# Kernel optimization log

Measured on AMD Instinct MI355X. Metric: run time of the kernel, lower is better.

## Reference

```python
import jax, jax.numpy as jnp
import numpy as np

B, CIN, NH, W, L, K = 16, 64, 64, 32, 4, 5
EPS = 1e-5
FORGET_BIAS = 1.0


def conv(x, w, b=None):
    # x: [B,C,H,W], w: [O,I,k,k] -> SAME padding, stride 1 (NCHW)
    y = jax.lax.conv_general_dilated(x, w, (1, 1), 'SAME',
                                     dimension_numbers=('NCHW', 'OIHW', 'NCHW'))
    if b is not None:
        y = y + b[None, :, None, None]
    return y


def ln(x, g, b):
    # torch LayerNorm([C,W,W]): normalize each sample over (C,H,W)
    m = jnp.mean(x, axis=(1, 2, 3), keepdims=True)
    v = jnp.mean((x - m) ** 2, axis=(1, 2, 3), keepdims=True)
    return (x - m) * jax.lax.rsqrt(v + EPS) * g[None] + b[None]


def attn_channel(q, kv):
    # q: [B,C,W,H], kv: [B,L,C,W,H]
    b, c, w, h = q.shape
    qf = q.reshape(b, c, w * h)                 # [B,C,HW]
    kf = kv.reshape(b, -1, w * h)               # [B,L*C,HW]
    a = jax.nn.softmax(jnp.einsum('bcp,blp->bcl', qf, kf), axis=2)  # [B,C,L*C]
    out = jnp.einsum('bcl,blp->bcp', a, kf)     # [B,C,HW]
    return out.reshape(b, c, w, h)


def attn_spatial(q, kv):
    # q: [B,C,W,H], kv: [B,L,C,W,H]
    b, c, w, h = q.shape
    qf = q.reshape(b, c, w * h).transpose(0, 2, 1)          # [B,HW,C]
    kf = kv.transpose(0, 1, 3, 4, 2).reshape(b, -1, c)      # [B,L*HW,C]
    a = jax.nn.softmax(jnp.einsum('bpc,bqc->bpq', qf, kf), axis=2)  # [B,HW,L*HW]
    out = jnp.einsum('bpq,bqc->bpc', a, kf)                 # [B,HW,C]
    return out.reshape(b, w, h, c).transpose(0, 3, 1, 2)


def setup_inputs() -> dict:
    key = jax.random.key(0)
    ks = iter(jax.random.split(key, 64))
    rn = lambda shape, s=1.0: jax.random.normal(next(ks), shape, jnp.float32) * s
    ones = lambda shape: jnp.ones(shape, jnp.float32)
    zeros = lambda shape: jnp.zeros(shape, jnp.float32)
    s = 0.02
    d = {}
    d['x_t'] = rn((B, CIN, W, W))
    d['h_t'] = rn((B, NH, W, W))
    d['c_t'] = rn((B, NH, W, W))
    d['c_historys'] = rn((B, L, NH, W, W))
    d['m_t'] = rn((B, NH, W, W))
    d['w_x'] = rn((7 * NH, CIN, K, K), s); d['ln_x_g'] = ones((7 * NH, W, W)); d['ln_x_b'] = zeros((7 * NH, W, W))
    d['w_h'] = rn((4 * NH, NH, K, K), s);  d['ln_h_g'] = ones((4 * NH, W, W)); d['ln_h_b'] = zeros((4 * NH, W, W))
    d['w_m'] = rn((3 * NH, NH, K, K), s);  d['ln_m_g'] = ones((3 * NH, W, W)); d['ln_m_b'] = zeros((3 * NH, W, W))
    d['w_o'] = rn((NH, 2 * NH, K, K), s);  d['ln_o_g'] = ones((NH, W, W));     d['ln_o_b'] = zeros((NH, W, W))
    d['w_last'] = rn((NH, 2 * NH, 1, 1), s)
    d['s_norm_g'] = ones((NH, W, W)); d['s_norm_b'] = zeros((NH, W, W))
    d['c_norm_g'] = ones((NH, W, W)); d['c_norm_b'] = zeros((NH, W, W))
    d['ca_w1'] = rn((NH, NH, K, K), s); d['ca_b1'] = zeros((NH,))
    d['ca_ln_g'] = ones((NH, W, W));    d['ca_ln_b'] = zeros((NH, W, W))
    d['ca_w2'] = rn((NH, NH, 1, 1), s); d['ca_b2'] = zeros((NH,))
    d['sa_w1'] = rn((NH, NH, K, K), s)
    d['sa_ln_g'] = ones((NH, W, W));    d['sa_ln_b'] = zeros((NH, W, W))
    d['sa_w2'] = rn((NH, NH, 1, 1), s)
    d['attn_w'] = rn((NH, NH, 1, 1), s)
    return d


def reference(x_t, h_t, c_t, c_historys, m_t,
              w_x, ln_x_g, ln_x_b, w_h, ln_h_g, ln_h_b, w_m, ln_m_g, ln_m_b,
              w_o, ln_o_g, ln_o_b, w_last,
              s_norm_g, s_norm_b, c_norm_g, c_norm_b,
              ca_w1, ca_b1, ca_ln_g, ca_ln_b, ca_w2, ca_b2,
              sa_w1, sa_ln_g, sa_ln_b, sa_w2, attn_w):
    x_concat = ln(conv(x_t, w_x), ln_x_g, ln_x_b)
    h_concat = ln(conv(h_t, w_h), ln_h_g, ln_h_b)
    m_concat = ln(conv(m_t, w_m), ln_m_g, ln_m_b)
    (i_x, f_x, g_x, i_xp, f_xp, g_xp, o_x) = jnp.split(x_concat, 7, axis=1)
    (i_h, f_h, g_h, o_h) = jnp.split(h_concat, 4, axis=1)
    (i_m, f_m, g_m) = jnp.split(m_concat, 3, axis=1)

    i_t = jax.nn.sigmoid(i_x + i_h)
    f_t = jax.nn.sigmoid(f_x + f_h + FORGET_BIAS)
    g_t = jnp.tanh(g_x + g_h)

    # attn_sum_fussion(c_t, query=f_t, keys=c_historys, values=c_historys)
    sp = ln(c_t + attn_spatial(f_t, c_historys), s_norm_g, s_norm_b)
    ch = ln(c_t + attn_channel(f_t, c_historys), c_norm_g, c_norm_b)
    s_a = conv(jax.nn.relu(ln(conv(sp, sa_w1), sa_ln_g, sa_ln_b)), sa_w2)
    c_a = conv(jax.nn.relu(ln(conv(ch, ca_w1, ca_b1), ca_ln_g, ca_ln_b)), ca_w2, ca_b2)
    attn = conv(s_a + c_a, attn_w)
    c_new = attn + i_t * g_t

    i_tp = jax.nn.sigmoid(i_xp + i_m)
    f_tp = jax.nn.sigmoid(f_xp + f_m + FORGET_BIAS)
    g_tp = jnp.tanh(g_xp + g_m)
    m_new = f_tp * m_t + i_tp * g_tp

    mem = jnp.concatenate((c_new, m_new), axis=1)
    o_t = jax.nn.sigmoid(o_x + o_h + ln(conv(mem, w_o), ln_o_g, ln_o_b))
    h_new = o_t * jnp.tanh(conv(mem, w_last))
    return h_new, c_new, m_new
```

## Files before the change

### kernel.cpp

```cpp
#include <hip/hip_runtime.h>
#include <hip/hip_bf16.h>

#define N1 (1u << 20)

typedef __attribute__((ext_vector_type(8))) short s8v;
typedef __attribute__((ext_vector_type(4))) float f4v;

static __device__ __forceinline__ float sigm(float x){ return 1.f/(1.f + __expf(-x)); }
static __device__ __forceinline__ float tanh_(float x){ return 1.f - 2.f/(__expf(2.f*x) + 1.f); }

static __device__ __forceinline__ ushort f2b(float f){
  union { float f; uint u; } x; x.f = f;
  uint r = x.u + 0x7FFFu + ((x.u >> 16) & 1u);
  return (ushort)(r >> 16);
}

static __device__ __forceinline__ void red_atomic2(float s, float q, float* d, int b, int t){
  #pragma unroll
  for (int m = 32; m; m >>= 1){ s += __shfl_xor(s, m); q += __shfl_xor(q, m); }
  if ((t & 63) == 0){ atomicAdd(&d[b*2], s); atomicAdd(&d[b*2+1], q); }
}

__global__ void k_zero(float* __restrict__ p){ p[threadIdx.x] = 0.f; }

__global__ __launch_bounds__(256) void k_wprep3(
    const float* __restrict__ sA, ushort* __restrict__ dA, int CoA, int CiA, int nA,
    const float* __restrict__ sB, ushort* __restrict__ dB, int CoB, int CiB, int nB,
    const float* __restrict__ sC, ushort* __restrict__ dC, int CoC, int CiC, int nC)
{
  int idx = blockIdx.x*256 + threadIdx.x;
  const float* s; ushort* d; int Co, Ci;
  if (idx < nA){ s=sA; d=dA; Co=CoA; Ci=CiA; }
  else if ((idx -= nA) < nB){ s=sB; d=dB; Co=CoB; Ci=CiB; }
  else if ((idx -= nB) < nC){ s=sC; d=dC; Co=CoC; Ci=CiC; }
  else return;
  const int ci32 = idx & 31;
  const int r  = idx >> 5;
  const int co = r % Co;
  const int r2 = r / Co;
  const int tap = r2 % 25, cc = r2 / 25;
  d[idx] = f2b(s[((size_t)(co*Ci + (cc<<5) + ci32))*25 + tap]);
}

struct PT { const float* s; ushort* d; const float* st; const float* g; const float* bb; };

__global__ __launch_bounds__(256) void k_prepT3(PT ja, PT jb, PT jc, int n0, int n1, float invN)
{
  const int lp = blockIdx.y;
  PT j; int pl;
  if (lp < n0){ j = ja; pl = lp; }
  else if (lp < n0 + n1){ j = jb; pl = lp - n0; }
  else { j = jc; pl = lp - n0 - n1; }
  const float* sp = j.s + ((size_t)pl << 16);
  float mean = 0.f, rstd = 0.f;
  if (j.st){
    float s0 = j.st[pl*2], s1 = j.st[pl*2+1];
    mean = s0*invN; rstd = rsqrtf(s1*invN - mean*mean + 1e-5f);
  }
  const int p0 = blockIdx.x << 6;
  __shared__ __align__(16) float T[64][68];
  const int t = threadIdx.x, c = t >> 2, g4 = t & 3;
  #pragma unroll
  for (int i = 0; i < 4; ++i){
    const int px = (g4 << 4) + (i << 2);
    float4 f = *(const float4*)(sp + ((size_t)c << 10) + p0 + px);
    if (j.st){
      const size_t li = ((size_t)c << 10) + p0 + px;
      float4 gv = *(const float4*)(j.g + li);
      float4 bv = *(const float4*)(j.bb + li);
      f.x = (f.x - mean)*rstd*gv.x + bv.x;
      f.y = (f.y - mean)*rstd*gv.y + bv.y;
      f.z = (f.z - mean)*rstd*gv.z + bv.z;
      f.w = (f.w - mean)*rstd*gv.w + bv.w;
    }
    *(float4*)&T[c][px] = f;
  }
  __syncthreads();
  const int p = t >> 2, c0 = (t & 3) << 4;
  uint w4[8];
  #pragma unroll
  for (int k = 0; k < 8; ++k){
    ushort lo = f2b(T[c0 + 2*k][p]);
    ushort hi = f2b(T[c0 + 2*k + 1][p]);
    w4[k] = (uint)lo | ((uint)hi << 16);
  }
  ushort* dst = j.d + ((((size_t)pl << 10) + p0 + p) << 6) + c0;
  *(uint4*)(dst)     = *(uint4*)&w4[0];
  *(uint4*)(dst + 8) = *(uint4*)&w4[4];
}

__global__ __launch_bounds__(256) void k_prepTm(const float* __restrict__ src, ushort* __restrict__ dT)
{
  const int lp = blockIdx.y;
  const int p0 = blockIdx.x << 6;
  const float* sp = src + ((size_t)lp << 16);
  __shared__ __align__(16) float T[64][68];
  const int t = threadIdx.x, c = t >> 2, g4 = t & 3;
  #pragma unroll
  for (int i = 0; i < 4; ++i){
    const int px = (g4 << 4) + (i << 2);
    *(float4*)&T[c][px] = *(const float4*)(sp + ((size_t)c << 10) + p0 + px);
  }
  __syncthreads();
  const int p = t >> 2, c0 = (t & 3) << 4;
  uint w4[8];
  #pragma unroll
  for (int k = 0; k < 8; ++k)
    w4[k] = (uint)f2b(T[c0 + 2*k][p]) | ((uint)f2b(T[c0 + 2*k + 1][p]) << 16);
  ushort* dst = dT + ((((size_t)(lp >> 1) << 10) + p0 + p) << 7) + ((lp & 1) << 6) + c0;
  *(uint4*)(dst)     = *(uint4*)&w4[0];
  *(uint4*)(dst + 8) = *(uint4*)&w4[4];
}

struct Seg {
  const ushort* inT; const ushort* w; const float* bias;
  float* out; float* ostat;
  int Cin, Cout;
};
struct Segs3 { Seg s[3]; int b1, b2; };

template<int MT>
__global__ __launch_bounds__(256, MT==4 ? 3 : 4) void k_convX(Segs3 Sg)
{
  constexpr int CO = MT*16;
  const int b = blockIdx.y;
  const int cog = blockIdx.x >> 2, pxblk = blockIdx.x & 3;
  const int si = (cog >= Sg.b1) + (cog >= Sg.b2);
  const Seg sg = Sg.s[si];
  const int base = si == 0 ? 0 : (si == 1 ? Sg.b1 : Sg.b2);
  const int co0 = (cog - base) * CO;
  const int r0 = pxblk << 3;
  const int t = threadIdx.x, w = t >> 6, l = t & 63;
  const int lane16 = l & 15, quad = l >> 4;
  const int lofs = (lane16 << 5) + (quad << 3);

  __shared__ __align__(16) ushort S_[4][12][36][8];

  f4v acc[MT][4];
  #pragma unroll
  for (int mi = 0; mi < MT; ++mi)
    #pragma unroll
    for (int n = 0; n < 4; ++n) acc[mi][n] = (f4v){0.f,0.f,0.f,0.f};

  const int ncc = sg.Cin >> 5;
  for (int cc = 0; cc < ncc; ++cc){
    __syncthreads();
    for (int idx = t; idx < 432; idx += 256){
      const int row = idx / 36, col = idx - row*36;
      const int ir = r0 - 2 + row, ic = col - 2;
      uint4 pk[4] = {make_uint4(0,0,0,0),make_uint4(0,0,0,0),make_uint4(0,0,0,0),make_uint4(0,0,0,0)};
      if ((unsigned)ir < 32u && (unsigned)ic < 32u){
        const ushort* bp = sg.inT + ((size_t)((b << 10) + (ir << 5) + ic)) * sg.Cin + (cc << 5);
        #pragma unroll
        for (int q = 0; q < 4; ++q) pk[q] = *(const uint4*)(bp + (q << 3));
      }
      #pragma unroll
      for (int q = 0; q < 4; ++q) *(uint4*)&S_[q][row][col][0] = pk[q];
    }
    __syncthreads();
    #pragma unroll
    for (int dy = 0; dy < 5; ++dy){
      #pragma unroll
      for (int dx = 0; dx < 5; ++dx){
        const ushort* wp = sg.w + (((size_t)((cc*25 + dy*5 + dx)*sg.Cout + co0)) << 5) + lofs;
        s8v a[MT];
        #pragma unroll
        for (int mi = 0; mi < MT; ++mi)
          a[mi] = *(const s8v*)(wp + mi*512);
        #pragma unroll
        for (int n = 0; n < 4; ++n){
          const int srow = (w << 1) + (n >> 1) + dy;
          const int col = ((n & 1) << 4) + lane16 + dx;
          s8v bb = *(const s8v*)&S_[quad][srow][col][0];
          #pragma unroll
          for (int mi = 0; mi < MT; ++mi)
            acc[mi][n] = __builtin_amdgcn_mfma_f32_16x16x32_bf16(a[mi], bb, acc[mi][n], 0, 0, 0);
        }
      }
    }
  }
  float lsum = 0.f, lsq = 0.f;
  #pragma unroll
  for (int mi = 0; mi < MT; ++mi){
    const int co = co0 + mi*16 + (quad << 2);
    #pragma unroll
    for (int n = 0; n < 4; ++n){
      const int row = r0 + (w << 1) + (n >> 1);
      const int col = ((n & 1) << 4) + lane16;
      #pragma unroll
      for (int i = 0; i < 4; ++i){
        float v = acc[mi][n][i] + (sg.bias ? sg.bias[co+i] : 0.f);
        sg.out[(((size_t)(b*sg.Cout + co + i)) << 10) + (row << 5) + col] = v;
        lsum += v; lsq += v*v;
      }
    }
  }
  if (sg.ostat) red_atomic2(lsum, lsq, sg.ostat, b, t);
}

__global__ __launch_bounds__(256) void k_prep(const float* __restrict__ src,
                                              ushort* __restrict__ outC,
                                              ushort* __restrict__ outT)
{
  const int plane = blockIdx.y;
  const int p0 = blockIdx.x << 6;
  const float* sp = src + ((size_t)plane << 16);
  __shared__ __align__(16) float T[64][68];
  const int t = threadIdx.x, c = t >> 2, g = t & 3;
  #pragma unroll
  for (int i = 0; i < 4; ++i){
    float4 f = *(const float4*)(sp + ((size_t)c << 10) + p0 + (g << 4) + (i << 2));
    *(float4*)&T[c][(g << 4) + (i << 2)] = f;
    if (outC){
      uint2 pk2;
      pk2.x = (uint)f2b(f.x) | ((uint)f2b(f.y) << 16);
      pk2.y = (uint)f2b(f.z) | ((uint)f2b(f.w) << 16);
      *(uint2*)(outC + ((((size_t)plane << 6) + c) << 10) + p0 + (g << 4) + (i << 2)) = pk2;
    }
  }
  __syncthreads();
  const int p = t >> 2, c0 = (t & 3) << 4;
  uint w4[8];
  #pragma unroll
  for (int k = 0; k < 8; ++k){
    ushort lo = f2b(T[c0 + 2*k][p]);
    ushort hi = f2b(T[c0 + 2*k + 1][p]);
    w4[k] = (uint)lo | ((uint)hi << 16);
  }
  ushort* dst = outT + ((((size_t)plane << 10) + p0 + p) << 6) + c0;
  *(uint4*)(dst)     = *(uint4*)&w4[0];
  *(uint4*)(dst + 8) = *(uint4*)&w4[4];
}

__global__ __launch_bounds__(256) void k_gates(
    const float* __restrict__ bufx, const float* __restrict__ bufh, const float* __restrict__ bufm,
    const float* __restrict__ lnxg, const float* __restrict__ lnxb,
    const float* __restrict__ lnhg, const float* __restrict__ lnhb,
    const float* __restrict__ lnmg, const float* __restrict__ lnmb,
    const float* __restrict__ m_t, const float* __restrict__ stats,
    float* __restrict__ ft, float* __restrict__ ig, float* __restrict__ osum,
    float* __restrict__ memo, float* __restrict__ out_m)
{
  const int idx = blockIdx.x*256 + threadIdx.x;
  const int b = idx >> 16, rem = idx & 65535;
  const int c = rem >> 10, p = rem & 1023;

  float mx = stats[b*2]      * (1.f/458752.f);
  float vx = stats[b*2+1]    * (1.f/458752.f) - mx*mx;  float rx = rsqrtf(vx + 1e-5f);
  float mh = stats[32+b*2]   * (1.f/262144.f);
  float vh = stats[32+b*2+1] * (1.f/262144.f) - mh*mh;  float rh = rsqrtf(vh + 1e-5f);
  float mm = stats[64+b*2]   * (1.f/196608.f);
  float vm = stats[64+b*2+1] * (1.f/196608.f) - mm*mm;  float rm = rsqrtf(vm + 1e-5f);

  auto LX = [&](int k){
    size_t ch = (size_t)k*64 + c; size_t gi = ((size_t)b*448 + ch)*1024 + p; size_t li = ch*1024 + p;
    return (bufx[gi] - mx)*rx*lnxg[li] + lnxb[li]; };
  auto LH = [&](int k){
    size_t ch = (size_t)k*64 + c; size_t gi = ((size_t)b*256 + ch)*1024 + p; size_t li = ch*1024 + p;
    return (bufh[gi] - mh)*rh*lnhg[li] + lnhb[li]; };
  auto LM = [&](int k){
    size_t ch = (size_t)k*64 + c; size_t gi = ((size_t)b*192 + ch)*1024 + p; size_t li = ch*1024 + p;
    return (bufm[gi] - mm)*rm*lnmg[li] + lnmb[li]; };

  float i_t = sigm(LX(0) + LH(0));
  float f_t = sigm(LX(1) + LH(1) + 1.f);
  float g_t = tanh_(LX(2) + LH(2));
  float i_p = sigm(LX(3) + LM(0));
  float f_p = sigm(LX(4) + LM(1) + 1.f);
  float g_p = tanh_(LX(5) + LM(2));
  float ox = LX(6), oh = LH(3);

  ft[idx]   = f_t;
  ig[idx]   = i_t * g_t;
  osum[idx] = ox + oh;
  float mn = f_p * m_t[idx] + i_p * g_p;
  out_m[idx] = mn;
  memo[((size_t)(b*128 + 64 + c) << 10) + p] = mn;
}

__global__ __launch_bounds__(256) void k_spat_mfma(
    const ushort* __restrict__ qT, const ushort* __restrict__ kvC, const ushort* __restrict__ kvT,
    const float* __restrict__ c_t, float* __restrict__ sp_raw, float* __restrict__ stats)
{
  const int p0 = blockIdx.x << 6, b = blockIdx.y;
  const int t = threadIdx.x, w = t >> 6, l = t & 63;
  const int lane16 = l & 15, quad = l >> 4;
  __shared__ __align__(16) ushort Kt[64][72];
  __shared__ __align__(16) ushort Kc[64][72];
  __shared__ __align__(16) ushort Eb[64][72];
  __shared__ __align__(16) float  XO[64][65];

  s8v qa0, qa1;
  {
    const ushort* qr = qT + ((((size_t)b << 10) + p0 + (w << 4) + lane16) << 6) + (quad << 3);
    qa0 = *(const s8v*)(qr);
    qa1 = *(const s8v*)(qr + 32);
  }
  f4v o0 = {0.f,0.f,0.f,0.f}, o1 = o0, o2 = o0, o3 = o0, dacc = o0;
  const short oneb = (short)0x3F80;
  const s8v ones = { oneb, oneb, oneb, oneb, oneb, oneb, oneb, oneb };

  const int r = t >> 2, g4 = (t & 3) << 4;
  for (int chunk = 0; chunk < 64; ++chunk){
    const int lidx = chunk >> 4, pk = (chunk & 15) << 6;
    __syncthreads();
    {
      const ushort* sc = kvC + ((((size_t)(b*4 + lidx) << 6) + r) << 10) + pk + g4;
      *(uint4*)&Kc[r][g4]     = *(const uint4*)(sc);
      *(uint4*)&Kc[r][g4 + 8] = *(const uint4*)(sc + 8);
      const ushort* st = kvT + ((((size_t)(b*4 + lidx) << 10) + pk + r) << 6) + g4;
      *(uint4*)&Kt[r][g4]     = *(const uint4*)(st);
      *(uint4*)&Kt[r][g4 + 8] = *(const uint4*)(st + 8);
    }
    __syncthreads();
    #pragma unroll
    for (int nt = 0; nt < 4; ++nt){
      const ushort* bt = &Kt[(nt << 4) + lane16][quad << 3];
      s8v b0 = *(const s8v*)(bt);
      s8v b1 = *(const s8v*)(bt + 32);
      f4v s = {0.f,0.f,0.f,0.f};
      s = __builtin_amdgcn_mfma_f32_16x16x32_bf16(qa0, b0, s, 0, 0, 0);
      s = __builtin_amdgcn_mfma_f32_16x16x32_bf16(qa1, b1, s, 0, 0, 0);
      #pragma unroll
      for (int i = 0; i < 4; ++i){
        float e = __expf(s[i] - 12.f);
        Eb[(w << 4) + (quad << 2) + i][(nt << 4) + lane16] = f2b(e);
      }
    }
    __syncthreads();
    #pragma unroll
    for (int ks = 0; ks < 2; ++ks){
      s8v ea = *(const s8v*)&Eb[(w << 4) + lane16][(ks << 5) + (quad << 3)];
      dacc = __builtin_amdgcn_mfma_f32_16x16x32_bf16(ea, ones, dacc, 0, 0, 0);
      s8v bc0 = *(const s8v*)&Kc[ 0 + lane16][(ks << 5) + (quad << 3)];
      s8v bc1 = *(const s8v*)&Kc[16 + lane16][(ks << 5) + (quad << 3)];
      s8v bc2 = *(const s8v*)&Kc[32 + lane16][(ks << 5) + (quad << 3)];
      s8v bc3 = *(const s8v*)&Kc[48 + lane16][(ks << 5) + (quad << 3)];
      o0 = __builtin_amdgcn_mfma_f32_16x16x32_bf16(ea, bc0, o0, 0, 0, 0);
      o1 = __builtin_amdgcn_mfma_f32_16x16x32_bf16(ea, bc1, o1, 0, 0, 0);
      o2 = __builtin_amdgcn_mfma_f32_16x16x32_bf16(ea, bc2, o2, 0, 0, 0);
// ... 229 lines not shown
  float acc2[4][4] = {};
  for (int c2 = 0; c2 < 64; ++c2){
    float wv[4], mv[4];
    *(float4*)wv = *(const float4*)&Wl[c2][4*tc];
    *(float4*)mv = *(const float4*)&Ms[c2][4*tp];
    #pragma unroll
    for (int i = 0; i < 4; ++i)
      #pragma unroll
      for (int j = 0; j < 4; ++j)
        acc2[i][j] = fmaf(wv[i], mv[j], acc2[i][j]);
  }
  #pragma unroll
  for (int i = 0; i < 4; ++i)
    #pragma unroll
    for (int j = 0; j < 4; ++j){
      size_t gi = ((size_t)b << 16) + ((size_t)(4*tc + i) << 10) + p0 + 4*tp + j;
      float v = acc2[i][j] + ig[gi];
      out_c[gi] = v;
      memo[((size_t)(b*128 + 4*tc + i) << 10) + p0 + 4*tp + j] = v;
    }
}

__global__ __launch_bounds__(256) void k_final(
    const float* __restrict__ memo, const float* __restrict__ wlast,
    const float* __restrict__ bufo, const float* __restrict__ osum,
    const float* __restrict__ stats_o, const float* __restrict__ lnog, const float* __restrict__ lnob,
    float* __restrict__ out_h)
{
  const int p0 = blockIdx.x << 6, b = blockIdx.y, t = threadIdx.x;
  const int tc = t & 15, tp = t >> 4;
  __shared__ __align__(16) float Msh[64][68];
  __shared__ __align__(16) float Wt[64][68];
  float acc[4][4] = {};
  #pragma unroll
  for (int half = 0; half < 2; ++half){
    __syncthreads();
    {
      const int j = t & 63, c0 = t >> 6;
      for (int ci = c0; ci < 64; ci += 4)
        Msh[ci][j] = memo[((size_t)(b*128 + half*64 + ci) << 10) + p0 + j];
      const int ci2 = t & 63, co0 = t >> 6;
      for (int co = co0; co < 64; co += 4) Wt[ci2][co] = wlast[((size_t)co << 7) + half*64 + ci2];
    }
    __syncthreads();
    for (int ci = 0; ci < 64; ++ci){
      float wv[4], mv[4];
      *(float4*)wv = *(const float4*)&Wt[ci][4*tc];
      *(float4*)mv = *(const float4*)&Msh[ci][4*tp];
      #pragma unroll
      for (int i = 0; i < 4; ++i)
        #pragma unroll
        for (int j = 0; j < 4; ++j)
          acc[i][j] = fmaf(wv[i], mv[j], acc[i][j]);
    }
  }
  float mean = stats_o[b*2]*(1.f/65536.f);
  float var  = stats_o[b*2+1]*(1.f/65536.f) - mean*mean;
  float rstd = rsqrtf(var + 1e-5f);
  #pragma unroll
  for (int i = 0; i < 4; ++i)
    #pragma unroll
    for (int j = 0; j < 4; ++j){
      const int co = 4*tc + i, p = p0 + 4*tp + j;
      size_t gi = ((size_t)b << 16) + ((size_t)co << 10) + p;
      size_t li = ((size_t)co << 10) + p;
      float lno = (bufo[gi] - mean)*rstd*lnog[li] + lnob[li];
      float o = sigm(osum[gi] + lno);
      out_h[gi] = o * tanh_(acc[i][j]);
    }
}

extern "C" void kernel_launch(void* const* d_in, const int* in_sizes, int n_in,
                              void* d_out, int out_size, void* d_ws, size_t ws_size,
                              hipStream_t stream)
{
  const float* x_t   = (const float*)d_in[0];
  const float* h_t   = (const float*)d_in[1];
  const float* c_t   = (const float*)d_in[2];
  const float* chist = (const float*)d_in[3];
  const float* m_t   = (const float*)d_in[4];
  const float* w_x   = (const float*)d_in[5];
  const float* lnxg  = (const float*)d_in[6];
  const float* lnxb  = (const float*)d_in[7];
  const float* w_h   = (const float*)d_in[8];
  const float* lnhg  = (const float*)d_in[9];
  const float* lnhb  = (const float*)d_in[10];
  const float* w_m   = (const float*)d_in[11];
  const float* lnmg  = (const float*)d_in[12];
  const float* lnmb  = (const float*)d_in[13];
  const float* w_o   = (const float*)d_in[14];
  const float* lnog  = (const float*)d_in[15];
  const float* lnob  = (const float*)d_in[16];
  const float* w_last= (const float*)d_in[17];
  const float* sng   = (const float*)d_in[18];
  const float* snb   = (const float*)d_in[19];
  const float* cng   = (const float*)d_in[20];
  const float* cnb   = (const float*)d_in[21];
  const float* ca_w1 = (const float*)d_in[22];
  const float* ca_b1 = (const float*)d_in[23];
  const float* calng = (const float*)d_in[24];
  const float* calnb = (const float*)d_in[25];
  const float* ca_w2 = (const float*)d_in[26];
  const float* ca_b2 = (const float*)d_in[27];
  const float* sa_w1 = (const float*)d_in[28];
  const float* salng = (const float*)d_in[29];
  const float* salnb = (const float*)d_in[30];
  const float* sa_w2 = (const float*)d_in[31];
  const float* attn_w= (const float*)d_in[32];

  float* out = (float*)d_out;
  float* ws  = (float*)d_ws;

  float* stats = ws;
  float* bufx  = ws + 1024;
  float* bufh  = bufx + 7*(size_t)N1;
  float* bufm  = bufh + 4*(size_t)N1;
  float* ft    = bufm + 3*(size_t)N1;
  float* ig    = ft   + (size_t)N1;
  float* osum  = ig   + (size_t)N1;
  float* memo  = osum + (size_t)N1;
  float* sp    = bufx;
  float* ch    = bufx + (size_t)N1;
  float* samid = bufx + 2*(size_t)N1;
  float* camid = bufx + 3*(size_t)N1;
  float* bufo  = bufx + 4*(size_t)N1;
  float* chl   = bufx + 5*(size_t)N1;
  ushort* kvC  = (ushort*)bufh;
  ushort* kvT  = kvC + 4*(size_t)N1;
  ushort* qT   = (ushort*)bufm;
  ushort* ftC  = qT + (size_t)N1;

  ushort* xT   = (ushort*)memo;
  ushort* hT   = xT + (size_t)N1;
  ushort* mT   = hT + (size_t)N1;
  ushort* spT  = ftC + (size_t)N1;
  ushort* chT  = spT + (size_t)N1;
  ushort* memoT = (ushort*)bufx;

  ushort* wbx = (ushort*)ft;
  ushort* wbh = wbx + 716800;
  ushort* wbm = wbh + 409600;
  ushort* wbo  = (ushort*)(chl + 262144);
  ushort* wbsa = wbo + 204800;
  ushort* wbca = wbsa + 102400;
  ushort* chlb = wbca + 102400;

  float* out_h = out;
  float* out_c = out + (size_t)N1;
  float* out_m = out + 2*(size_t)N1;

  k_zero<<<dim3(1), dim3(256), 0, stream>>>(stats);

  k_wprep3<<<dim3(5600), dim3(256), 0, stream>>>(
      w_x, wbx, 448, 64, 716800,
      w_h, wbh, 256, 64, 409600,
      w_m, wbm, 192, 64, 307200);

  {
    PT jx{ x_t, xT, nullptr, nullptr, nullptr };
    PT jh{ h_t, hT, nullptr, nullptr, nullptr };
    PT jm{ m_t, mT, nullptr, nullptr, nullptr };
    k_prepT3<<<dim3(16,48), dim3(256), 0, stream>>>(jx, jh, jm, 16, 16, 0.f);
  }

  {
    Segs3 XHM;
    XHM.s[0] = Seg{ xT, wbx, nullptr, bufx, stats+0,  64, 448 };
    XHM.s[1] = Seg{ hT, wbh, nullptr, bufh, stats+32, 64, 256 };
    XHM.s[2] = Seg{ mT, wbm, nullptr, bufm, stats+64, 64, 192 };
    XHM.b1 = 7; XHM.b2 = 11;
    k_convX<4><<<dim3(56,16), dim3(256), 0, stream>>>(XHM);
  }

  k_gates<<<dim3(4096), dim3(256), 0, stream>>>(bufx, bufh, bufm, lnxg, lnxb, lnhg, lnhb,
                                                lnmg, lnmb, m_t, stats,
                                                ft, ig, osum, memo, out_m);

  k_wprep3<<<dim3(1600), dim3(256), 0, stream>>>(
      w_o,   wbo,  64, 128, 204800,
      sa_w1, wbsa, 64,  64, 102400,
      ca_w1, wbca, 64,  64, 102400);

  k_prep<<<dim3(16,64), dim3(256), 0, stream>>>(chist, kvC, kvT);
  k_prep<<<dim3(16,16), dim3(256), 0, stream>>>(ft, ftC, qT);

  k_spat_mfma<<<dim3(16,16), dim3(256), 0, stream>>>(qT, kvC, kvT, c_t, sp, stats+96);
  k_chlog_m<<<dim3(2,16), dim3(256), 0, stream>>>(ftC, kvC, chl);
  k_chsm  <<<dim3(256),  dim3(256), 0, stream>>>(chl, chlb);
  k_chout_m<<<dim3(8,16), dim3(256), 0, stream>>>(chlb, kvT, c_t, ch, stats+128);

  {
    PT js{ sp, spT, stats+96,  sng, snb };
    PT jc{ ch, chT, stats+128, cng, cnb };
    k_prepT3<<<dim3(16,32), dim3(256), 0, stream>>>(js, jc, js, 16, 16, 1.f/65536.f);
  }

  {
    Segs3 SC;
    SC.s[0] = Seg{ spT, wbsa, nullptr, samid, stats+160, 64, 64 };
    SC.s[1] = Seg{ chT, wbca, ca_b1,   camid, stats+192, 64, 64 };
    SC.s[2] = SC.s[1];
    SC.b1 = 2; SC.b2 = 1000;
    k_convX<2><<<dim3(16,16), dim3(256), 0, stream>>>(SC);
  }

  k_attnfinal<<<dim3(16,16), dim3(256), 0, stream>>>(samid, camid, stats+160, stats+192,
                                                     salng, salnb, calng, calnb,
                                                     sa_w2, ca_w2, ca_b2, attn_w,
                                                     ig, out_c, memo);

  k_prepTm<<<dim3(16,32), dim3(256), 0, stream>>>(memo, memoT);

  {
    Segs3 O;
    O.s[0] = Seg{ memoT, wbo, nullptr, bufo, stats+224, 128, 64 };
    O.s[1] = O.s[0]; O.s[2] = O.s[0];
    O.b1 = 1000; O.b2 = 1000;
    k_convX<2><<<dim3(8,16), dim3(256), 0, stream>>>(O);
  }

  k_final<<<dim3(16,16), dim3(256), 0, stream>>>(memo, w_last, bufo, osum, stats+224,
                                                 lnog, lnob, out_h);
}
```

Measured before the change: 550.6 us.

## Stage conv weights through double-buffered LDS with register prefetch per kernel row

Conv weights are now stored as [tap][Cout][Cin] instead of the chunked layout. Each dy row's weights for the block's output channels are cooperatively loaded into a double-buffered shared-memory tile, and the next row is prefetched into registers while MFMAs run on the current one. This replaces per-wave direct global weight loads, which several waves repeated, with shared LDS reads. In exchange it adds a __syncthreads per dy row and more LDS and register use, and the launch-bounds occupancy hint is lowered to match.

```diff
diff --git a/kernel.cpp b/kernel.cpp
--- a/kernel.cpp
+++ b/kernel.cpp
@@ -34,12 +34,8 @@
   else if ((idx -= nA) < nB){ s=sB; d=dB; Co=CoB; Ci=CiB; }
   else if ((idx -= nB) < nC){ s=sC; d=dC; Co=CoC; Ci=CiC; }
   else return;
-  const int ci32 = idx & 31;
-  const int r  = idx >> 5;
-  const int co = r % Co;
-  const int r2 = r / Co;
-  const int tap = r2 % 25, cc = r2 / 25;
-  d[idx] = f2b(s[((size_t)(co*Ci + (cc<<5) + ci32))*25 + tap]);
+  int ci = idx % Ci; int r = idx / Ci; int co = r % Co; int tap = r / Co;
+  d[idx] = f2b(s[((size_t)(co*Ci + ci))*25 + tap]);
 }
 
 struct PT { const float* s; ushort* d; const float* st; const float* g; const float* bb; };
@@ -120,9 +116,13 @@
 struct Segs3 { Seg s[3]; int b1, b2; };
 
 template<int MT>
-__global__ __launch_bounds__(256, MT==4 ? 3 : 4) void k_convX(Segs3 Sg)
-{
-  constexpr int CO = MT*16;
+__global__ __launch_bounds__(256, MT==4 ? 2 : 3) void k_convX(Segs3 Sg)
+{
+  constexpr int CO   = MT*16;
+  constexpr int NW   = 5*CO*4;
+  constexpr int ITW  = (NW + 255) / 256;
+  constexpr int DXSH = (MT == 4 ? 8 : 7);
+
   const int b = blockIdx.y;
   const int cog = blockIdx.x >> 2, pxblk = blockIdx.x & 3;
   const int si = (cog >= Sg.b1) + (cog >= Sg.b2);
@@ -132,15 +132,25 @@
   const int r0 = pxblk << 3;
   const int t = threadIdx.x, w = t >> 6, l = t & 63;
   const int lane16 = l & 15, quad = l >> 4;
-  const int lofs = (lane16 << 5) + (quad << 3);
 
   __shared__ __align__(16) ushort S_[4][12][36][8];
+  __shared__ __align__(16) ushort W_[2][5*CO*32];
 
   f4v acc[MT][4];
   #pragma unroll
   for (int mi = 0; mi < MT; ++mi)
     #pragma unroll
     for (int n = 0; n < 4; ++n) acc[mi][n] = (f4v){0.f,0.f,0.f,0.f};
+
+  size_t woff0[ITW];
+  #pragma unroll
+  for (int it = 0; it < ITW; ++it){
+    const int u = t + it*256;
+    const int l16u = u & 15, qu = (u >> 4) & 3;
+    const int miu = (u >> 6) & (MT - 1), dxu = u >> DXSH;
+    woff0[it] = ((size_t)(dxu*sg.Cout + co0 + miu*16 + l16u))*sg.Cin + (qu << 3);
+  }
+  const size_t wdy = (size_t)5 * sg.Cout * sg.Cin;
 
   const int ncc = sg.Cin >> 5;
   for (int cc = 0; cc < ncc; ++cc){
@@ -157,16 +167,35 @@
       #pragma unroll
       for (int q = 0; q < 4; ++q) *(uint4*)&S_[q][row][col][0] = pk[q];
     }
+    {
+      uint4 wreg[ITW];
+      #pragma unroll
+      for (int it = 0; it < ITW; ++it)
+        if (ITW*256 == NW || t + it*256 < NW)
+          wreg[it] = *(const uint4*)(sg.w + woff0[it] + (cc << 5));
+      #pragma unroll
+      for (int it = 0; it < ITW; ++it)
+        if (ITW*256 == NW || t + it*256 < NW)
+          *(uint4*)&W_[0][(size_t)(t + it*256) * 8] = wreg[it];
+    }
     __syncthreads();
     #pragma unroll
     for (int dy = 0; dy < 5; ++dy){
+      uint4 nreg[ITW];
+      if (dy < 4){
+        #pragma unroll
+        for (int it = 0; it < ITW; ++it)
+          if (ITW*256 == NW || t + it*256 < NW)
+            nreg[it] = *(const uint4*)(sg.w + woff0[it] + (size_t)(dy+1)*wdy + (cc << 5));
+      }
       #pragma unroll
       for (int dx = 0; dx < 5; ++dx){
-        const ushort* wp = sg.w + (((size_t)((cc*25 + dy*5 + dx)*sg.Cout + co0)) << 5) + lofs;
         s8v a[MT];
         #pragma unroll
-        for (int mi = 0; mi < MT; ++mi)
-          a[mi] = *(const s8v*)(wp + mi*512);
+        for (int mi = 0; mi < MT; ++mi){
+          const int au = ((((dx*MT + mi) << 2) + quad) << 4) + lane16;
+          a[mi] = *(const s8v*)&W_[dy & 1][au << 3];
+        }
         #pragma unroll
         for (int n = 0; n < 4; ++n){
           const int srow = (w << 1) + (n >> 1) + dy;
@@ -177,6 +206,13 @@
             acc[mi][n] = __builtin_amdgcn_mfma_f32_16x16x32_bf16(a[mi], bb, acc[mi][n], 0, 0, 0);
         }
       }
+      if (dy < 4){
+        #pragma unroll
+        for (int it = 0; it < ITW; ++it)
+          if (ITW*256 == NW || t + it*256 < NW)
+            *(uint4*)&W_[(dy+1) & 1][(size_t)(t + it*256) * 8] = nreg[it];
+      }
+      __syncthreads();
     }
   }
   float lsum = 0.f, lsq = 0.f;
```

New measurement: 519.0 us. -5.7%, faster.

## Re-layout conv weights and activations, prefetch weight fragments, split small convs finer

Applied to the files above, without the earlier changes.

Weights are now packed per output-channel tile with taps innermost, so each block reads a contiguous region. Activations are stored in 8-channel group planes, which makes each LDS fill a single 16-byte load per unit. The conv loop double-buffers the A (weight) fragments one tap ahead to hide global-load latency behind the MFMAs. The smaller convs use 4 rows per block, doubling the grid to improve occupancy at the cost of more halo reloads. This rests on a new layout contract between the prep kernels and the conv kernel, and every consumer of these buffers must agree with it.

```diff
diff --git a/kernel.cpp b/kernel.cpp
--- a/kernel.cpp
+++ b/kernel.cpp
@@ -24,22 +24,28 @@
 __global__ void k_zero(float* __restrict__ p){ p[threadIdx.x] = 0.f; }
 
 __global__ __launch_bounds__(256) void k_wprep3(
-    const float* __restrict__ sA, ushort* __restrict__ dA, int CoA, int CiA, int nA,
-    const float* __restrict__ sB, ushort* __restrict__ dB, int CoB, int CiB, int nB,
-    const float* __restrict__ sC, ushort* __restrict__ dC, int CoC, int CiC, int nC)
+    const float* __restrict__ sA, ushort* __restrict__ dA, int CoA, int CiA, int COA, int nA,
+    const float* __restrict__ sB, ushort* __restrict__ dB, int CoB, int CiB, int COB, int nB,
+    const float* __restrict__ sC, ushort* __restrict__ dC, int CoC, int CiC, int COC, int nC)
 {
   int idx = blockIdx.x*256 + threadIdx.x;
-  const float* s; ushort* d; int Co, Ci;
-  if (idx < nA){ s=sA; d=dA; Co=CoA; Ci=CiA; }
-  else if ((idx -= nA) < nB){ s=sB; d=dB; Co=CoB; Ci=CiB; }
-  else if ((idx -= nB) < nC){ s=sC; d=dC; Co=CoC; Ci=CiC; }
+  const float* s; ushort* d; int Co, Ci, CO;
+  if (idx < nA){ s=sA; d=dA; Co=CoA; Ci=CiA; CO=COA; }
+  else if ((idx -= nA) < nB){ s=sB; d=dB; Co=CoB; Ci=CiB; CO=COB; }
+  else if ((idx -= nB) < nC){ s=sC; d=dC; Co=CoC; Ci=CiC; CO=COC; }
   else return;
-  const int ci32 = idx & 31;
-  const int r  = idx >> 5;
-  const int co = r % Co;
-  const int r2 = r / Co;
-  const int tap = r2 % 25, cc = r2 / 25;
-  d[idx] = f2b(s[((size_t)(co*Ci + (cc<<5) + ci32))*25 + tap]);
+  const int ci8 = idx & 7;
+  int u = idx >> 3;
+  const int q = u & 3; u >>= 2;
+  const int cl = u % CO; u /= CO;
+  const int dx = u % 5;  u /= 5;
+  const int dy = u % 5;  u /= 5;
+  const int nCot = Co / CO;
+  const int cot = u % nCot;
+  const int cc  = u / nCot;
+  const int co = cot*CO + cl;
+  const int ci = (cc << 5) + (q << 3) + ci8;
+  d[idx] = f2b(s[((size_t)(co*Ci + ci))*25 + dy*5 + dx]);
 }
 
 struct PT { const float* s; ushort* d; const float* st; const float* g; const float* bb; };
@@ -84,9 +90,11 @@
     ushort hi = f2b(T[c0 + 2*k + 1][p]);
     w4[k] = (uint)lo | ((uint)hi << 16);
   }
-  ushort* dst = j.d + ((((size_t)pl << 10) + p0 + p) << 6) + c0;
-  *(uint4*)(dst)     = *(uint4*)&w4[0];
-  *(uint4*)(dst + 8) = *(uint4*)&w4[4];
+  const int q0 = c0 >> 3;
+  ushort* d0 = j.d + ((((size_t)pl*8 + q0    ) << 10) + p0 + p)*8;
+  ushort* d1 = j.d + ((((size_t)pl*8 + q0 + 1) << 10) + p0 + p)*8;
+  *(uint4*)d0 = *(uint4*)&w4[0];
+  *(uint4*)d1 = *(uint4*)&w4[4];
 }
 
 __global__ __launch_bounds__(256) void k_prepTm(const float* __restrict__ src, ushort* __restrict__ dT)
@@ -107,9 +115,11 @@
   #pragma unroll
   for (int k = 0; k < 8; ++k)
     w4[k] = (uint)f2b(T[c0 + 2*k][p]) | ((uint)f2b(T[c0 + 2*k + 1][p]) << 16);
-  ushort* dst = dT + ((((size_t)(lp >> 1) << 10) + p0 + p) << 7) + ((lp & 1) << 6) + c0;
-  *(uint4*)(dst)     = *(uint4*)&w4[0];
-  *(uint4*)(dst + 8) = *(uint4*)&w4[4];
+  const int b = lp >> 1, q0 = ((lp & 1) << 3) + (c0 >> 3);
+  ushort* d0 = dT + ((((size_t)b*16 + q0    ) << 10) + p0 + p)*8;
+  ushort* d1 = dT + ((((size_t)b*16 + q0 + 1) << 10) + p0 + p)*8;
+  *(uint4*)d0 = *(uint4*)&w4[0];
+  *(uint4*)d1 = *(uint4*)&w4[4];
 }
 
 struct Seg {
@@ -119,64 +129,89 @@
 };
 struct Segs3 { Seg s[3]; int b1, b2; };
 
-template<int MT>
+template<int MT, int RPB>
 __global__ __launch_bounds__(256, MT==4 ? 3 : 4) void k_convX(Segs3 Sg)
 {
-  constexpr int CO = MT*16;
+  constexpr int CO   = MT*16;
+  constexpr int PXB  = 32/RPB;
+  constexpr int ROWS = RPB + 4;
+  constexpr int RPW  = RPB/4;
+  constexpr int NTIL = RPB/2;
+  constexpr int SUNITS = 4*ROWS*36;
+
   const int b = blockIdx.y;
-  const int cog = blockIdx.x >> 2, pxblk = blockIdx.x & 3;
+  const int cog = blockIdx.x / PXB, pxblk = blockIdx.x % PXB;
   const int si = (cog >= Sg.b1) + (cog >= Sg.b2);
   const Seg sg = Sg.s[si];
   const int base = si == 0 ? 0 : (si == 1 ? Sg.b1 : Sg.b2);
-  const int co0 = (cog - base) * CO;
-  const int r0 = pxblk << 3;
+  const int cot = cog - base;
+  const int co0 = cot * CO;
+  const int r0 = pxblk * RPB;
   const int t = threadIdx.x, w = t >> 6, l = t & 63;
   const int lane16 = l & 15, quad = l >> 4;
-  const int lofs = (lane16 << 5) + (quad << 3);
-
-  __shared__ __align__(16) ushort S_[4][12][36][8];
-
-  f4v acc[MT][4];
+
+  __shared__ __align__(16) ushort S_[4][ROWS][36][8];
+
+  f4v acc[MT][NTIL];
   #pragma unroll
   for (int mi = 0; mi < MT; ++mi)
     #pragma unroll
-    for (int n = 0; n < 4; ++n) acc[mi][n] = (f4v){0.f,0.f,0.f,0.f};
+    for (int n = 0; n < NTIL; ++n) acc[mi][n] = (f4v){0.f,0.f,0.f,0.f};
+
+  const int nCot = sg.Cout / CO;
+  const size_t ccstr = (size_t)nCot * 5 * CO * 160;
+  const ushort* wct = sg.w + (size_t)cot * 5 * CO * 160;
+  const int lofs = lane16*32 + quad*8;
+
+  auto LDA = [&](int cc_, int dy_, int dx_, int mi_) -> s8v {
+    return *(const s8v*)(wct + (size_t)cc_*ccstr + dy_*(CO*160) + (dx_*CO + mi_*16)*32 + lofs);
+  };
 
   const int ncc = sg.Cin >> 5;
+  const int ngrp = sg.Cin >> 3;
+
+  s8v aC[MT], aN[MT];
+  #pragma unroll
+  for (int mi = 0; mi < MT; ++mi) aC[mi] = LDA(0, 0, 0, mi);
+
   for (int cc = 0; cc < ncc; ++cc){
-    __syncthreads();
-    for (int idx = t; idx < 432; idx += 256){
-      const int row = idx / 36, col = idx - row*36;
+    if (cc) __syncthreads();
+    for (int idx = t; idx < SUNITS; idx += 256){
+      const int q   = idx / (ROWS*36);
+      const int rem = idx - q*(ROWS*36);
+      const int row = rem / 36, col = rem - row*36;
       const int ir = r0 - 2 + row, ic = col - 2;
-      uint4 pk[4] = {make_uint4(0,0,0,0),make_uint4(0,0,0,0),make_uint4(0,0,0,0),make_uint4(0,0,0,0)};
+      uint4 pk = make_uint4(0,0,0,0);
       if ((unsigned)ir < 32u && (unsigned)ic < 32u){
-        const ushort* bp = sg.inT + ((size_t)((b << 10) + (ir << 5) + ic)) * sg.Cin + (cc << 5);
+        const ushort* bp = sg.inT + ((((size_t)(b*ngrp + (cc<<2) + q)) << 10) + (ir<<5) + ic)*8;
+        pk = *(const uint4*)bp;
+      }
+      *(uint4*)&S_[q][row][col][0] = pk;
+    }
+    __syncthreads();
+    #pragma unroll
+    for (int tp = 0; tp < 25; ++tp){
+      const int dy = tp/5, dx = tp - dy*5;
+      if (tp < 24){
+        const int ntp = tp + 1, ndy = ntp/5, ndx = ntp - ndy*5;
         #pragma unroll
-        for (int q = 0; q < 4; ++q) pk[q] = *(const uint4*)(bp + (q << 3));
-      }
-      #pragma unroll
-      for (int q = 0; q < 4; ++q) *(uint4*)&S_[q][row][col][0] = pk[q];
-    }
-    __syncthreads();
-    #pragma unroll
-    for (int dy = 0; dy < 5; ++dy){
-      #pragma unroll
-      for (int dx = 0; dx < 5; ++dx){
-        const ushort* wp = sg.w + (((size_t)((cc*25 + dy*5 + dx)*sg.Cout + co0)) << 5) + lofs;
-        s8v a[MT];
+        for (int mi = 0; mi < MT; ++mi) aN[mi] = LDA(cc, ndy, ndx, mi);
+      } else {
+        const int ccn = (cc + 1 < ncc) ? cc + 1 : cc;
+        #pragma unroll
+        for (int mi = 0; mi < MT; ++mi) aN[mi] = LDA(ccn, 0, 0, mi);
+      }
+      #pragma unroll
+      for (int n = 0; n < NTIL; ++n){
+        const int srow = w*RPW + (n>>1) + dy;
+        const int col  = ((n&1)<<4) + lane16 + dx;
+        s8v bb = *(const s8v*)&S_[quad][srow][col][0];
         #pragma unroll
         for (int mi = 0; mi < MT; ++mi)
-          a[mi] = *(const s8v*)(wp + mi*512);
-        #pragma unroll
-        for (int n = 0; n < 4; ++n){
-          const int srow = (w << 1) + (n >> 1) + dy;
-          const int col = ((n & 1) << 4) + lane16 + dx;
-          s8v bb = *(const s8v*)&S_[quad][srow][col][0];
-          #pragma unroll
-          for (int mi = 0; mi < MT; ++mi)
-            acc[mi][n] = __builtin_amdgcn_mfma_f32_16x16x32_bf16(a[mi], bb, acc[mi][n], 0, 0, 0);
-        }
-      }
+          acc[mi][n] = __builtin_amdgcn_mfma_f32_16x16x32_bf16(aC[mi], bb, acc[mi][n], 0, 0, 0);
+      }
+      #pragma unroll
+      for (int mi = 0; mi < MT; ++mi) aC[mi] = aN[mi];
     }
   }
   float lsum = 0.f, lsq = 0.f;
@@ -184,8 +219,8 @@
   for (int mi = 0; mi < MT; ++mi){
     const int co = co0 + mi*16 + (quad << 2);
     #pragma unroll
-    for (int n = 0; n < 4; ++n){
-      const int row = r0 + (w << 1) + (n >> 1);
+    for (int n = 0; n < NTIL; ++n){
+      const int row = r0 + w*RPW + (n>>1);
       const int col = ((n & 1) << 4) + lane16;
       #pragma unroll
       for (int i = 0; i < 4; ++i){
@@ -721,9 +756,9 @@
   k_zero<<<dim3(1), dim3(256), 0, stream>>>(stats);
 
   k_wprep3<<<dim3(5600), dim3(256), 0, stream>>>(
-      w_x, wbx, 448, 64, 716800,
-      w_h, wbh, 256, 64, 409600,
-      w_m, wbm, 192, 64, 307200);
+      w_x, wbx, 448, 64, 64, 716800,
+      w_h, wbh, 256, 64, 64, 409600,
+      w_m, wbm, 192, 64, 64, 307200);
 
   {
     PT jx{ x_t, xT, nullptr, nullptr, nullptr };
@@ -738,7 +773,7 @@
     XHM.s[1] = Seg{ hT, wbh, nullptr, bufh, stats+32, 64, 256 };
     XHM.s[2] = Seg{ mT, wbm, nullptr, bufm, stats+64, 64, 192 };
     XHM.b1 = 7; XHM.b2 = 11;
-    k_convX<4><<<dim3(56,16), dim3(256), 0, stream>>>(XHM);
+    k_convX<4,8><<<dim3(56,16), dim3(256), 0, stream>>>(XHM);
   }
 
   k_gates<<<dim3(4096), dim3(256), 0, stream>>>(bufx, bufh, bufm, lnxg, lnxb, lnhg, lnhb,
@@ -746,9 +781,9 @@
                                                 ft, ig, osum, memo, out_m);
 
   k_wprep3<<<dim3(1600), dim3(256), 0, stream>>>(
-      w_o,   wbo,  64, 128, 204800,
-      sa_w1, wbsa, 64,  64, 102400,
-      ca_w1, wbca, 64,  64, 102400);
+      w_o,   wbo,  64, 128, 32, 204800,
+      sa_w1, wbsa, 64,  64, 32, 102400,
+      ca_w1, wbca, 64,  64, 32, 102400);
 
   k_prep<<<dim3(16,64), dim3(256), 0, stream>>>(chist, kvC, kvT);
   k_prep<<<dim3(16,16), dim3(256), 0, stream>>>(ft, ftC, qT);
@@ -770,7 +805,7 @@
     SC.s[1] = Seg{ chT, wbca, ca_b1,   camid, stats+192, 64, 64 };
     SC.s[2] = SC.s[1];
     SC.b1 = 2; SC.b2 = 1000;
-    k_convX<2><<<dim3(16,16), dim3(256), 0, stream>>>(SC);
+    k_convX<2,4><<<dim3(32,16), dim3(256), 0, stream>>>(SC);
   }
 
   k_attnfinal<<<dim3(16,16), dim3(256), 0, stream>>>(samid, camid, stats+160, stats+192,
@@ -785,7 +820,7 @@
     O.s[0] = Seg{ memoT, wbo, nullptr, bufo, stats+224, 128, 64 };
     O.s[1] = O.s[0]; O.s[2] = O.s[0];
     O.b1 = 1000; O.b2 = 1000;
-    k_convX<2><<<dim3(8,16), dim3(256), 0, stream>>>(O);
+    k_convX<2,4><<<dim3(16,16), dim3(256), 0, stream>>>(O);
   }
 
   k_final<<<dim3(16,16), dim3(256), 0, stream>>>(memo, w_last, bufo, osum, stats+224,
```

Result: no change. 542.5 us (-1.5%).

## Stage conv weights in LDS with register prefetch and rolling input-row buffer

Applied to the files above, without the earlier changes.

The conv kernel now stages each dy-row of weights into shared memory, prefetching the next row into registers while the current one computes, instead of reading weights straight from global memory per tap. The input tile becomes a ring of RPB rows that is refilled one row per dy step. Activation and weight layouts change to channel-group-major (8-channel groups) to match. Smaller conv launches get more pixel blocks through the new RPB template parameter. The cost is extra barriers per dy step and more shared memory.

```diff
diff --git a/kernel.cpp b/kernel.cpp
--- a/kernel.cpp
+++ b/kernel.cpp
@@ -34,12 +34,8 @@
   else if ((idx -= nA) < nB){ s=sB; d=dB; Co=CoB; Ci=CiB; }
   else if ((idx -= nB) < nC){ s=sC; d=dC; Co=CoC; Ci=CiC; }
   else return;
-  const int ci32 = idx & 31;
-  const int r  = idx >> 5;
-  const int co = r % Co;
-  const int r2 = r / Co;
-  const int tap = r2 % 25, cc = r2 / 25;
-  d[idx] = f2b(s[((size_t)(co*Ci + (cc<<5) + ci32))*25 + tap]);
+  int ci = idx % Ci; int r = idx / Ci; int co = r % Co; int tap = r / Co;
+  d[idx] = f2b(s[((size_t)(co*Ci + ci))*25 + tap]);
 }
 
 struct PT { const float* s; ushort* d; const float* st; const float* g; const float* bb; };
@@ -84,9 +80,11 @@
     ushort hi = f2b(T[c0 + 2*k + 1][p]);
     w4[k] = (uint)lo | ((uint)hi << 16);
   }
-  ushort* dst = j.d + ((((size_t)pl << 10) + p0 + p) << 6) + c0;
-  *(uint4*)(dst)     = *(uint4*)&w4[0];
-  *(uint4*)(dst + 8) = *(uint4*)&w4[4];
+  const int q0 = c0 >> 3;
+  ushort* d0 = j.d + ((((size_t)pl*8 + q0    ) << 10) + p0 + p)*8;
+  ushort* d1 = j.d + ((((size_t)pl*8 + q0 + 1) << 10) + p0 + p)*8;
+  *(uint4*)d0 = *(uint4*)&w4[0];
+  *(uint4*)d1 = *(uint4*)&w4[4];
 }
 
 __global__ __launch_bounds__(256) void k_prepTm(const float* __restrict__ src, ushort* __restrict__ dT)
@@ -107,9 +105,11 @@
   #pragma unroll
   for (int k = 0; k < 8; ++k)
     w4[k] = (uint)f2b(T[c0 + 2*k][p]) | ((uint)f2b(T[c0 + 2*k + 1][p]) << 16);
-  ushort* dst = dT + ((((size_t)(lp >> 1) << 10) + p0 + p) << 7) + ((lp & 1) << 6) + c0;
-  *(uint4*)(dst)     = *(uint4*)&w4[0];
-  *(uint4*)(dst + 8) = *(uint4*)&w4[4];
+  const int b = lp >> 1, q0 = ((lp & 1) << 3) + (c0 >> 3);
+  ushort* d0 = dT + ((((size_t)b*16 + q0    ) << 10) + p0 + p)*8;
+  ushort* d1 = dT + ((((size_t)b*16 + q0 + 1) << 10) + p0 + p)*8;
+  *(uint4*)d0 = *(uint4*)&w4[0];
+  *(uint4*)d1 = *(uint4*)&w4[4];
 }
 
 struct Seg {
@@ -119,64 +119,125 @@
 };
 struct Segs3 { Seg s[3]; int b1, b2; };
 
-template<int MT>
-__global__ __launch_bounds__(256, MT==4 ? 3 : 4) void k_convX(Segs3 Sg)
-{
-  constexpr int CO = MT*16;
+template<int MT, int RPB>
+__global__ __launch_bounds__(256, 4) void k_convX(Segs3 Sg)
+{
+  constexpr int CO   = MT*16;
+  constexpr int PXB  = 32/RPB;
+  constexpr int RPW  = RPB/4;
+  constexpr int NTIL = RPB/2;
+  constexpr int NWU  = 5*CO*4;
+  constexpr int ITW  = (NWU + 255)/256;
+  constexpr int DXSH = (MT == 4 ? 8 : 7);
+  constexpr int SBULK = 4*RPB*36;
+  constexpr int ITS  = (SBULK + 255)/256;
+
   const int b = blockIdx.y;
-  const int cog = blockIdx.x >> 2, pxblk = blockIdx.x & 3;
+  const int cog = blockIdx.x / PXB, pxblk = blockIdx.x % PXB;
   const int si = (cog >= Sg.b1) + (cog >= Sg.b2);
   const Seg sg = Sg.s[si];
   const int base = si == 0 ? 0 : (si == 1 ? Sg.b1 : Sg.b2);
   const int co0 = (cog - base) * CO;
-  const int r0 = pxblk << 3;
+  const int r0 = pxblk * RPB;
   const int t = threadIdx.x, w = t >> 6, l = t & 63;
   const int lane16 = l & 15, quad = l >> 4;
-  const int lofs = (lane16 << 5) + (quad << 3);
-
-  __shared__ __align__(16) ushort S_[4][12][36][8];
-
-  f4v acc[MT][4];
+
+  __shared__ __align__(16) ushort S_[4][RPB][36][8];
+  __shared__ __align__(16) ushort W_[NWU*8];
+
+  f4v acc[MT][NTIL];
   #pragma unroll
   for (int mi = 0; mi < MT; ++mi)
     #pragma unroll
-    for (int n = 0; n < 4; ++n) acc[mi][n] = (f4v){0.f,0.f,0.f,0.f};
-
-  const int ncc = sg.Cin >> 5;
+    for (int n = 0; n < NTIL; ++n) acc[mi][n] = (f4v){0.f,0.f,0.f,0.f};
+
+  const int ngrp = sg.Cin >> 3;
+  const int ncc  = sg.Cin >> 5;
+  const uint wdy = 5u * sg.Cout * sg.Cin;
+
+  uint woff0[ITW];
+  #pragma unroll
+  for (int it = 0; it < ITW; ++it){
+    const int u = t + it*256;
+    woff0[it] = (uint)((u>>DXSH)*sg.Cout + co0 + ((u>>6)&(MT-1))*16 + (u&15))*(uint)sg.Cin
+              + ((u>>4)&3)*8;
+  }
+  const int rq = t/36, rcol = t - rq*36;
+
+  uint4 wr[ITW];
+  auto issueW = [&](int cc_, int dy_){
+    #pragma unroll
+    for (int it = 0; it < ITW; ++it){
+      const int u = t + it*256;
+      if (ITW*256 == NWU || u < NWU)
+        wr[it] = *(const uint4*)(sg.w + (size_t)(woff0[it] + dy_*wdy + (cc_<<5)));
+    }
+  };
+  auto writeW = [&](){
+    #pragma unroll
+    for (int it = 0; it < ITW; ++it){
+      const int u = t + it*256;
+      if (ITW*256 == NWU || u < NWU)
+        *(uint4*)&W_[(size_t)u*8] = wr[it];
+    }
+  };
+
+  issueW(0, 0);
+
   for (int cc = 0; cc < ncc; ++cc){
-    __syncthreads();
-    for (int idx = t; idx < 432; idx += 256){
-      const int row = idx / 36, col = idx - row*36;
-      const int ir = r0 - 2 + row, ic = col - 2;
-      uint4 pk[4] = {make_uint4(0,0,0,0),make_uint4(0,0,0,0),make_uint4(0,0,0,0),make_uint4(0,0,0,0)};
-      if ((unsigned)ir < 32u && (unsigned)ic < 32u){
-        const ushort* bp = sg.inT + ((size_t)((b << 10) + (ir << 5) + ic)) * sg.Cin + (cc << 5);
-        #pragma unroll
-        for (int q = 0; q < 4; ++q) pk[q] = *(const uint4*)(bp + (q << 3));
-      }
-      #pragma unroll
-      for (int q = 0; q < 4; ++q) *(uint4*)&S_[q][row][col][0] = pk[q];
-    }
+    #pragma unroll
+    for (int it = 0; it < ITS; ++it){
+      const int idx = t + it*256;
+      if (ITS*256 == SBULK || idx < SBULK){
+        const int q = idx / (RPB*36);
+        const int rem = idx - q*(RPB*36);
+        const int s = rem / 36, col = rem - s*36;
+        const int ir = r0 - 2 + s, ic = col - 2;
+        uint4 pk = make_uint4(0,0,0,0);
+        if ((unsigned)ir < 32u && (unsigned)ic < 32u)
+          pk = *(const uint4*)(sg.inT + ((((size_t)(b*ngrp + (cc<<2) + q)) << 10) + (ir<<5) + ic)*8);
+        *(uint4*)&S_[q][s][col][0] = pk;
+      }
+    }
+    writeW();
+    issueW(cc, 1);
     __syncthreads();
     #pragma unroll
     for (int dy = 0; dy < 5; ++dy){
+      uint4 rowreg;
+      const bool rv = (dy < 4) && (t < 144);
+      if (rv){
+        const int ir = r0 - 2 + RPB + dy, ic = rcol - 2;
+        rowreg = make_uint4(0,0,0,0);
+        if ((unsigned)ir < 32u && (unsigned)ic < 32u)
+          rowreg = *(const uint4*)(sg.inT + ((((size_t)(b*ngrp + (cc<<2) + rq)) << 10) + (ir<<5) + ic)*8);
+      }
       #pragma unroll
       for (int dx = 0; dx < 5; ++dx){
-        const ushort* wp = sg.w + (((size_t)((cc*25 + dy*5 + dx)*sg.Cout + co0)) << 5) + lofs;
         s8v a[MT];
         #pragma unroll
-        for (int mi = 0; mi < MT; ++mi)
-          a[mi] = *(const s8v*)(wp + mi*512);
+        for (int mi = 0; mi < MT; ++mi){
+          const int au = ((dx*MT + mi)*4 + quad)*16 + lane16;
+          a[mi] = *(const s8v*)&W_[au*8];
+        }
         #pragma unroll
-        for (int n = 0; n < 4; ++n){
-          const int srow = (w << 1) + (n >> 1) + dy;
-          const int col = ((n & 1) << 4) + lane16 + dx;
-          s8v bb = *(const s8v*)&S_[quad][srow][col][0];
+        for (int n = 0; n < NTIL; ++n){
+          const int srow = w*RPW + (n>>1) + dy;
+          const int col  = ((n&1)<<4) + lane16 + dx;
+          s8v bb = *(const s8v*)&S_[quad][srow & (RPB-1)][col][0];
           #pragma unroll
           for (int mi = 0; mi < MT; ++mi)
             acc[mi][n] = __builtin_amdgcn_mfma_f32_16x16x32_bf16(a[mi], bb, acc[mi][n], 0, 0, 0);
         }
       }
+      __syncthreads();
+      if (dy < 4){
+        writeW();
+        if (dy == 3) issueW(cc + 1 < ncc ? cc + 1 : cc, 0);
+        else         issueW(cc, dy + 2);
+        if (rv) *(uint4*)&S_[rq][(RPB + dy) & (RPB-1)][rcol][0] = rowreg;
+        __syncthreads();
+      }
     }
   }
   float lsum = 0.f, lsq = 0.f;
@@ -184,8 +245,8 @@
   for (int mi = 0; mi < MT; ++mi){
     const int co = co0 + mi*16 + (quad << 2);
     #pragma unroll
-    for (int n = 0; n < 4; ++n){
-      const int row = r0 + (w << 1) + (n >> 1);
+    for (int n = 0; n < NTIL; ++n){
+      const int row = r0 + w*RPW + (n>>1);
       const int col = ((n & 1) << 4) + lane16;
       #pragma unroll
       for (int i = 0; i < 4; ++i){
@@ -738,7 +799,7 @@
     XHM.s[1] = Seg{ hT, wbh, nullptr, bufh, stats+32, 64, 256 };
     XHM.s[2] = Seg{ mT, wbm, nullptr, bufm, stats+64, 64, 192 };
     XHM.b1 = 7; XHM.b2 = 11;
-    k_convX<4><<<dim3(56,16), dim3(256), 0, stream>>>(XHM);
+    k_convX<4,8><<<dim3(56,16), dim3(256), 0, stream>>>(XHM);
   }
 
   k_gates<<<dim3(4096), dim3(256), 0, stream>>>(bufx, bufh, bufm, lnxg, lnxb, lnhg, lnhb,
@@ -770,7 +831,7 @@
     SC.s[1] = Seg{ chT, wbca, ca_b1,   camid, stats+192, 64, 64 };
     SC.s[2] = SC.s[1];
     SC.b1 = 2; SC.b2 = 1000;
-    k_convX<2><<<dim3(16,16), dim3(256), 0, stream>>>(SC);
+    k_convX<2,4><<<dim3(32,16), dim3(256), 0, stream>>>(SC);
   }
 
   k_attnfinal<<<dim3(16,16), dim3(256), 0, stream>>>(samid, camid, stats+160, stats+192,
@@ -785,7 +846,7 @@
     O.s[0] = Seg{ memoT, wbo, nullptr, bufo, stats+224, 128, 64 };
     O.s[1] = O.s[0]; O.s[2] = O.s[0];
     O.b1 = 1000; O.b2 = 1000;
-    k_convX<2><<<dim3(8,16), dim3(256), 0, stream>>>(O);
+    k_convX<2,4><<<dim3(16,16), dim3(256), 0, stream>>>(O);
   }
 
   k_final<<<dim3(16,16), dim3(256), 0, stream>>>(memo, w_last, bufo, osum, stats+224,
```

Result: slower. 592.2 us (+7.6%).
